# Performance work log

Hardware: AMD Instinct MI355X
Metric: run time of the kernel (lower is better)

The kernel has to match this reference:

```python
import jax, jax.numpy as jnp
import numpy as np

N_NODES = 100_000
N_EDGES = 1_600_000
N_FEAT = 11
HIDDEN = 128
N_GRAPHS = 4096


def gcn_conv(x, W, b, row, col, n_nodes):
    # PyG GCNConv (default): add self-loops, symmetric deg^-1/2 norm,
    # out[col] += norm * (x @ W)[row], then + bias.
    xw = x @ W  # [N, H]
    ew = jnp.ones(row.shape[0], dtype=xw.dtype)
    deg = jax.ops.segment_sum(ew, col, num_segments=n_nodes)
    dis = jnp.where(deg > 0, jax.lax.rsqrt(deg), 0.0).astype(xw.dtype)
    norm = dis[row] * dis[col]  # [E+N]
    msg = xw[row] * norm[:, None]  # gather + scale
    out = jax.ops.segment_sum(msg, col, num_segments=n_nodes)  # scatter-add
    return out + b


def setup_inputs() -> dict:
    key = jax.random.key(0)
    ks = jax.random.split(key, 12)
    x = jax.random.normal(ks[0], (N_NODES, N_FEAT), dtype=jnp.float32)
    edge_index = jax.random.randint(ks[1], (2, N_EDGES), 0, N_NODES, dtype=jnp.int64)
    batch = jnp.sort(jax.random.randint(ks[2], (N_NODES,), 0, N_GRAPHS, dtype=jnp.int64))

    def glorot(k, shape):
        lim = float(np.sqrt(6.0 / (shape[0] + shape[1])))
        return jax.random.uniform(k, shape, jnp.float32, -lim, lim)

    W1 = glorot(ks[3], (N_FEAT, HIDDEN))
    b1 = jnp.zeros((HIDDEN,), jnp.float32)
    W2 = glorot(ks[4], (HIDDEN, HIDDEN))
    b2 = jnp.zeros((HIDDEN,), jnp.float32)
    Wl1 = glorot(ks[5], (HIDDEN, HIDDEN))
    bl1 = jnp.zeros((HIDDEN,), jnp.float32)
    Wl2 = glorot(ks[6], (HIDDEN, 1))
    bl2 = jnp.zeros((1,), jnp.float32)
    return {"x": x, "W1": W1, "b1": b1, "W2": W2, "b2": b2,
            "Wl1": Wl1, "bl1": bl1, "Wl2": Wl2, "bl2": bl2,
            "edge_index": edge_index, "batch": batch}


def reference(x, W1, b1, W2, b2, Wl1, bl1, Wl2, bl2, edge_index, batch):
    n = x.shape[0]
    loops = jnp.arange(n, dtype=edge_index.dtype)
    row = jnp.concatenate([edge_index[0], loops])
    col = jnp.concatenate([edge_index[1], loops])

    h = jax.nn.relu(gcn_conv(x, W1, b1, row, col, n))
    h = jax.nn.relu(gcn_conv(h, W2, b2, row, col, n))

    # global_mean_pool over per-node graph ids
    sums = jax.ops.segment_sum(h, batch, num_segments=N_GRAPHS)
    cnts = jax.ops.segment_sum(jnp.ones((n,), h.dtype), batch, num_segments=N_GRAPHS)
    pooled = sums / jnp.maximum(cnts, 1.0)[:, None]  # [G, H]

    out = jax.nn.relu(pooled @ Wl1 + bl1) @ Wl2 + bl2  # [G, 1]
    return out
```

## Files before the change

### kernel.cpp

```cpp
#include <hip/hip_runtime.h>

#define NN 100000
#define NE 1600000
#define NF 11
#define HID 128
#define NG 4096
#define NB 391

#define BSH 7
#define BNODES 128
#define NBK 782
#define CAP 3072
#define EPB 8192
#define NBB 196

typedef short bf16x8 __attribute__((ext_vector_type(8)));
typedef float f32x4 __attribute__((ext_vector_type(4)));

__device__ __forceinline__ unsigned short f2bf(float f) {
    unsigned u = __float_as_uint(f);
    return (unsigned short)((u + 0x7FFFu + ((u >> 16) & 1u)) >> 16);
}
__device__ __forceinline__ unsigned packbf(float a, float b) {
    return (unsigned)f2bf(a) | ((unsigned)f2bf(b) << 16);
}
__device__ __forceinline__ float bflo(unsigned v) { return __uint_as_float(v << 16); }
__device__ __forceinline__ float bfhi(unsigned v) { return __uint_as_float(v & 0xFFFF0000u); }
__device__ __forceinline__ bf16x8 as_bf(uint4 u) { union { uint4 a; bf16x8 b; } v; v.a = u; return v.b; }

__global__ void k_zero(int* __restrict__ p, int n) {
    int i = blockIdx.x * blockDim.x + threadIdx.x;
    if (i < n) p[i] = 0;
}

__global__ __launch_bounds__(256) void k_bucket(const int* __restrict__ row, const int* __restrict__ col,
                                                int* __restrict__ bcur, int* __restrict__ staging) {
    __shared__ int cnt[NBK];
    __shared__ int loc[NBK];
    const int tid = threadIdx.x;
    const int e0 = blockIdx.x * EPB;
    for (int i = tid; i < NBK; i += 256) { cnt[i] = 0; loc[i] = 0; }
    __syncthreads();
    int rb[32]; unsigned pay[32];
#pragma unroll
    for (int j = 0; j < 32; ++j) {
        int e = e0 + j * 256 + tid;
        int c = (e < NE) ? col[e] : -1;
        int r = (e < NE) ? row[e] : 0;
        rb[j] = (c >= 0) ? (c >> BSH) : -1;
        pay[j] = (unsigned)r | ((unsigned)(c & (BNODES - 1)) << 17);
        if (rb[j] >= 0) atomicAdd(&cnt[rb[j]], 1);
    }
    __syncthreads();
    for (int b = tid; b < NBK; b += 256) {
        int c = cnt[b];
        cnt[b] = (c > 0) ? atomicAdd(&bcur[b], c) : 0;
    }
    __syncthreads();
#pragma unroll
    for (int j = 0; j < 32; ++j) {
        if (rb[j] >= 0) {
            int p = cnt[rb[j]] + atomicAdd(&loc[rb[j]], 1);
            staging[rb[j] * CAP + p] = (int)pay[j];
        }
    }
}

__global__ __launch_bounds__(256) void k_hist2(const int* __restrict__ staging, const int* __restrict__ bcur,
                                               int* __restrict__ degE, float* __restrict__ dis) {
    __shared__ int cnt[BNODES];
    const int b = blockIdx.x, tid = threadIdx.x;
    if (tid < BNODES) cnt[tid] = 0;
    __syncthreads();
    const int sz = bcur[b];
    const int base = b * CAP;
    for (int i = tid; i < sz; i += 256)
        atomicAdd(&cnt[((unsigned)staging[base + i]) >> 17], 1);
    __syncthreads();
    int n = b * BNODES + tid;
    if (tid < BNODES && n < NN) {
        int d = cnt[tid];
        degE[n] = d;
        dis[n] = rsqrtf((float)(d + 1));
    }
}

__global__ void k_scan1(const int* __restrict__ degE, int* __restrict__ startp, int* __restrict__ partial) {
    __shared__ int sh[256];
    int t = threadIdx.x, i = blockIdx.x * 256 + t;
    int v = (i < NN) ? degE[i] : 0;
    sh[t] = v; __syncthreads();
    for (int off = 1; off < 256; off <<= 1) {
        int u = (t >= off) ? sh[t - off] : 0; __syncthreads();
        sh[t] += u; __syncthreads();
    }
    if (i < NN) startp[i] = sh[t] - v;
    if (t == 255) partial[blockIdx.x] = sh[255];
}

__global__ void k_scan2(int* __restrict__ partial) {
    __shared__ int sh[512];
    int t = threadIdx.x;
    int v = (t < NB) ? partial[t] : 0;
    sh[t] = v; __syncthreads();
    for (int off = 1; off < 512; off <<= 1) {
        int u = (t >= off) ? sh[t - off] : 0; __syncthreads();
        sh[t] += u; __syncthreads();
    }
    if (t < NB) partial[t] = sh[t] - v;
}

__global__ void k_scan3(int* __restrict__ startp, const int* __restrict__ partial) {
    int i = blockIdx.x * 256 + threadIdx.x;
    if (i < NN) startp[i] += partial[blockIdx.x];
    if (i == 0) startp[NN] = NE;
}

__global__ __launch_bounds__(256) void k_fillb(const int* __restrict__ staging, const int* __restrict__ bcur,
                                               const int* __restrict__ startp, int* __restrict__ csr) {
    __shared__ int cur[BNODES];
    const int b = blockIdx.x, tid = threadIdx.x;
    int n = b * BNODES + tid;
    if (tid < BNODES) cur[tid] = (n < NN) ? startp[n] : 0;
    __syncthreads();
    const int sz = bcur[b];
    const int base = b * CAP;
    for (int i = tid; i < sz; i += 256) {
        unsigned p = (unsigned)staging[base + i];
        int pos = atomicAdd(&cur[p >> 17], 1);
        csr[pos] = (int)(p & 0x1FFFF);
    }
}

__global__ void k_w2t(const float* __restrict__ W2, unsigned* __restrict__ w2t) {
    int i = blockIdx.x * 256 + threadIdx.x;
    if (i >= HID * 64) return;
    int col = i >> 6, kw = i & 63;
    w2t[col * 64 + kw] = packbf(W2[(2 * kw) * HID + col], W2[(2 * kw + 1) * HID + col]);
}

__global__ __launch_bounds__(256) void k_xd(const float* __restrict__ x, const float* __restrict__ dis,
                                            unsigned* __restrict__ xd8) {
    const int n = blockIdx.x * 16 + (threadIdx.x >> 4);
    const int lane = threadIdx.x & 15;
    float f = (lane < NF) ? x[(size_t)n * NF + lane] : 0.f;
    f *= dis[n];
    float g = __shfl_down(f, 1, 16);
    if ((lane & 1) == 0 && lane < NF)
        xd8[n * 8 + (lane >> 1)] = packbf(f, g);
}

__global__ __launch_bounds__(256) void k_gat1(const unsigned* __restrict__ xd8,
                                              const int* __restrict__ startp,
                                              const int* __restrict__ csr,
                                              float2* __restrict__ aggf2) {
    const int node = blockIdx.x * 4 + (threadIdx.x >> 6);
    const int lane = threadIdx.x & 63;
    const int g = lane >> 3, f = lane & 7;
    const int s = startp[node], e = startp[node + 1];
    float ax = 0.f, ay = 0.f;
    for (int i = s; i < e; i += 64) {
        int idx = (i + lane < e) ? csr[i + lane] : 0;
        int m = e - i;
#pragma unroll
        for (int t = 0; t < 8; ++t) {
            if (t * 8 >= m) break;
            int r = __shfl(idx, t * 8 + g);
            unsigned v = ((t * 8 + g) < m && f < 6) ? xd8[r * 8 + f] : 0u;
            ax += bflo(v); ay += bfhi(v);
        }
    }
    ax += __shfl_xor(ax, 8);  ay += __shfl_xor(ay, 8);
    ax += __shfl_xor(ax, 16); ay += __shfl_xor(ay, 16);
    ax += __shfl_xor(ax, 32); ay += __shfl_xor(ay, 32);
    if (g == 0 && f < 6) {
        unsigned sv = xd8[node * 8 + f];
        aggf2[node * 8 + f] = make_float2(ax + bflo(sv), ay + bfhi(sv));
    }
}

__global__ __launch_bounds__(256) void k_xw1agg(const float2* __restrict__ aggf2, const float* __restrict__ W1,
                                                const float* __restrict__ dis, const float* __restrict__ b1,
                                                unsigned* __restrict__ hb) {
    __shared__ float w1s[NF * HID];
    __shared__ float xs[16 * 16];
    const int tid = threadIdx.x;
    const int n0 = blockIdx.x * 16;
    for (int i = tid; i < NF * HID; i += 256) w1s[i] = W1[i];
    if (tid < 128) {
        int nl = tid >> 3, l = tid & 7;
        if (l < 6) {
            float2 v = aggf2[(size_t)(n0 + nl) * 8 + l];
            xs[nl * 16 + 2 * l] = v.x;
            xs[nl * 16 + 2 * l + 1] = v.y;
        } else {
            xs[nl * 16 + 2 * l] = 0.f;
            xs[nl * 16 + 2 * l + 1] = 0.f;
        }
    }
    __syncthreads();
    const int f2 = tid & 63, sub = tid >> 6;
    float2 bb = ((const float2*)b1)[f2];
#pragma unroll
    for (int p = 0; p < 4; ++p) {
        int nl = p * 4 + sub;
        float s0 = 0.f, s1 = 0.f;
#pragma unroll
        for (int k = 0; k < NF; ++k) {
            float xv = xs[nl * 16 + k];
            s0 = fmaf(xv, w1s[k * HID + f2 * 2], s0);
            s1 = fmaf(xv, w1s[k * HID + f2 * 2 + 1], s1);
        }
        int n = n0 + nl;
        float d = dis[n];
        float ax = fmaxf(fmaf(s0, d, bb.x), 0.f);
        float ay = fmaxf(fmaf(s1, d, bb.y), 0.f);
        hb[n * 64 + f2] = packbf(ax, ay);
    }
}

__global__ __launch_bounds__(256) void k_xw2m(const unsigned* __restrict__ hb,
                                              const unsigned* __restrict__ w2t,
                                              const float* __restrict__ dis,
                                              unsigned* __restrict__ yb) {
    const int tid = threadIdx.x;
    const int wid = tid >> 6, lane = tid & 63;
    const int lr = lane & 15, lk = lane >> 4;
    const int n0 = blockIdx.x * 64;
    const int colb = wid * 32;
    const uint4* h4 = (const uint4*)hb;
    const uint4* w4 = (const uint4*)w2t;

    bf16x8 Bf[2][4];
#pragma unroll
    for (int c = 0; c < 2; ++c)
#pragma unroll
        for (int ks = 0; ks < 4; ++ks)
            Bf[c][ks] = as_bf(w4[(colb + c * 16 + lr) * 16 + ks * 4 + lk]);

    f32x4 acc[4][2];
#pragma unroll
    for (int r = 0; r < 4; ++r)
#pragma unroll
        for (int c = 0; c < 2; ++c) {
            f32x4 z = {0.f, 0.f, 0.f, 0.f};
            acc[r][c] = z;
        }

#pragma unroll
    for (int ks = 0; ks < 4; ++ks) {
        bf16x8 Af[4];
#pragma unroll
        for (int r = 0; r < 4; ++r)
            Af[r] = as_bf(h4[(size_t)(n0 + r * 16 + lr) * 16 + ks * 4 + lk]);
#pragma unroll
        for (int r = 0; r < 4; ++r)
#pragma unroll
            for (int c = 0; c < 2; ++c)
                acc[r][c] = __builtin_amdgcn_mfma_f32_16x16x32_bf16(Af[r], Bf[c][ks], acc[r][c], 0, 0, 0);
    }

#pragma unroll
    for (int r = 0; r < 4; ++r) {
#pragma unroll
        for (int i = 0; i < 4; ++i) {
            int nd = n0 + r * 16 + lk * 4 + i;
            float d = (nd < NN) ? dis[nd] : 0.f;
#pragma unroll
            for (int c = 0; c < 2; ++c) {
                float v = acc[r][c][i] * d;
                float o = __shfl_xor(v, 1);
                if (!(lane & 1) && nd < NN) {
                    int col = colb + c * 16 + lr;
                    yb[nd * 64 + (col >> 1)] = packbf(v, o);
                }
            }
        }
    }
}

__global__ __launch_bounds__(256) void k_gather(const unsigned* __restrict__ yb,
                                                const int* __restrict__ startp,
                                                const int* __restrict__ csr_rows,
                                                const float* __restrict__ dis,
                                                const float* __restrict__ b,
                                                unsigned* __restrict__ hb) {
    const int node = blockIdx.x * 4 + (threadIdx.x >> 6);
    const int lane = threadIdx.x & 63;
    int s = startp[node], e = startp[node + 1];
    unsigned sv = yb[node * 64 + lane];
    float ax = bflo(sv), ay = bfhi(sv);
    for (int i = s; i < e; i += 64) {
        int idx = (i + lane < e) ? csr_rows[i + lane] : 0;
        int m = min(64, e - i);
        int j = 0;
        for (; j + 7 < m; j += 8) {
            unsigned v[8];
#pragma unroll
            for (int u = 0; u < 8; ++u) {
                int r = __shfl(idx, j + u);
                v[u] = yb[r * 64 + lane];
            }
#pragma unroll
            for (int u = 0; u < 8; ++u) { ax += bflo(v[u]); ay += bfhi(v[u]); }
        }
        for (; j + 3 < m; j += 4) {
            unsigned v[4];
#pragma unroll
            for (int u = 0; u < 4; ++u) {
                int r = __shfl(idx, j + u);
                v[u] = yb[r * 64 + lane];
            }
#pragma unroll
            for (int u = 0; u < 4; ++u) { ax += bflo(v[u]); ay += bfhi(v[u]); }
        }
        for (; j < m; ++j) {
            int r = __shfl(idx, j);
            unsigned v = yb[r * 64 + lane];
            ax += bflo(v); ay += bfhi(v);
        }
    }
    float d = dis[node];
    float2 bb = ((const float2*)b)[lane];
    ax = fmaxf(fmaf(ax, d, bb.x), 0.f);
    ay = fmaxf(fmaf(ay, d, bb.y), 0.f);
    hb[node * 64 + lane] = packbf(ax, ay);
}

__global__ void k_bounds(const int* __restrict__ batch, int* __restrict__ gs) {
    int g = blockIdx.x * blockDim.x + threadIdx.x;
    if (g > NG) return;
    int lo = 0, hi = NN;
    while (lo < hi) {
        int mid = (lo + hi) >> 1;
        if (batch[mid] < g) lo = mid + 1; else hi = mid;
    }
    gs[g] = lo;
}

__global__ __launch_bounds__(64) void k_pool(const unsigned* __restrict__ hb, const int* __restrict__ gs,
                                             float* __restrict__ pooled) {
    int g = blockIdx.x, f2 = threadIdx.x;
    int s = gs[g], e = gs[g + 1];
    float ax = 0.f, ay = 0.f;
    for (int n = s; n < e; ++n) {
        unsigned v = hb[(size_t)n * 64 + f2];
        ax += bflo(v); ay += bfhi(v);
    }
    float inv = 1.0f / (float)max(e - s, 1);
    pooled[(size_t)g * HID + f2 * 2] = ax * inv;
    pooled[(size_t)g * HID + f2 * 2 + 1] = ay * inv;
}

__global__ __launch_bounds__(128) void k_head(const float* __restrict__ pooled,
                                              const float* __restrict__ Wl1, const float* __restrict__ bl1,
                                              const float* __restrict__ Wl2, const float* __restrict__ bl2,
                                              float* __restrict__ out) {
    __shared__ float p[HID];
    __shared__ float red[128];
    const int g = blockIdx.x, f = threadIdx.x;
    p[f] = pooled[(size_t)g * HID + f];
    __syncthreads();
    float s = bl1[f];
    for (int k = 0; k < HID; ++k) s = fmaf(p[k], Wl1[k * HID + f], s);
    s = fmaxf(s, 0.f);
    red[f] = s * Wl2[f];
    __syncthreads();
    for (int off = 64; off > 0; off >>= 1) {
        if (f < off) red[f] += red[f + off];
        __syncthreads();
    }
    if (f == 0) out[g] = red[0] + bl2[0];
}

extern "C" void kernel_launch(void* const* d_in, const int* in_sizes, int n_in,
                              void* d_out, int out_size, void* d_ws, size_t ws_size,
                              hipStream_t stream) {
    const float* x   = (const float*)d_in[0];
    const float* W1  = (const float*)d_in[1];
    const float* b1  = (const float*)d_in[2];
    const float* W2  = (const float*)d_in[3];
    const float* b2  = (const float*)d_in[4];
    const float* Wl1 = (const float*)d_in[5];
    const float* bl1 = (const float*)d_in[6];
    const float* Wl2 = (const float*)d_in[7];
    const float* bl2 = (const float*)d_in[8];
    const int* ei    = (const int*)d_in[9];
    const int* batch = (const int*)d_in[10];
    float* out = (float*)d_out;

    const int* row = ei;
    const int* col = ei + NE;

    char* ws = (char*)d_ws;
    size_t off = 0;
    unsigned* yb   = (unsigned*)(ws + off); off += (size_t)NN * 64 * 4;
    unsigned* hb   = (unsigned*)(ws + off); off += (size_t)NN * 64 * 4;
    unsigned* xd8  = (unsigned*)(ws + off); off += (size_t)NN * 8 * 4;
    float2* aggf2  = (float2*)  (ws + off); off += (size_t)NN * 8 * 8;
    int*   degE    = (int*)  (ws + off); off += (size_t)NN * 4;
    float* dis     = (float*)(ws + off); off += (size_t)NN * 4;
    int*   startp  = (int*)  (ws + off); off += (size_t)(NN + 1) * 4;
    int*   partial = (int*)  (ws + off); off += 512 * 4;
    int*   csr     = (int*)  (ws + off); off += (size_t)NE * 4;
    int*   gs      = (int*)  (ws + off); off += (size_t)(NG + 1) * 4;
    float* pooled  = (float*)(ws + off); off += (size_t)NG * HID * 4;
    int*   bcur    = (int*)  (ws + off); off += (size_t)NBK * 4;
    unsigned* w2t  = (unsigned*)(ws + off); off += (size_t)HID * 64 * 4;
    int*   staging = (int*)hb;

    k_zero<<<(NBK + 255) / 256, 256, 0, stream>>>(bcur, NBK);
    k_bucket<<<NBB, 256, 0, stream>>>(row, col, bcur, staging);
    k_hist2<<<NBK, 256, 0, stream>>>(staging, bcur, degE, dis);
    k_scan1<<<NB, 256, 0, stream>>>(degE, startp, partial);
    k_scan2<<<1, 512, 0, stream>>>(partial);
    k_scan3<<<NB, 256, 0, stream>>>(startp, partial);
    k_fillb<<<NBK, 256, 0, stream>>>(staging, bcur, startp, csr);
    k_bounds<<<(NG + 256) / 256, 256, 0, stream>>>(batch, gs);
    k_w2t<<<(HID * 64 + 255) / 256, 256, 0, stream>>>(W2, w2t);

    k_xd<<<NN / 16, 256, 0, stream>>>(x, dis, xd8);
    k_gat1<<<NN / 4, 256, 0, stream>>>(xd8, startp, csr, aggf2);
    k_xw1agg<<<NN / 16, 256, 0, stream>>>(aggf2, W1, dis, b1, hb);

    k_xw2m<<<(NN + 63) / 64, 256, 0, stream>>>(hb, w2t, dis, yb);
    k_gather<<<NN / 4, 256, 0, stream>>>(yb, startp, csr, dis, b2, hb);

    k_pool<<<NG, 64, 0, stream>>>(hb, gs, pooled);
    k_head<<<NG, 128, 0, stream>>>(pooled, Wl1, bl1, Wl2, bl2, out);
}
```

Before: 234.6 us.

## Slice layer-2 features into 8 column slabs for cache-friendly edge gather

The layer-2 message buffer is stored as eight feature slices of 16 columns each (32 bytes per node per slice). The gather now launches eight blocks per node group, one per slice, and each wave handles eight edges at a time with 8 lanes per edge. The intent is to shrink the random-access working set per slice so it fits in L2/MALL, at the cost of reading the CSR indices eight times and issuing 8x more blocks. Layer-1's gather drops its early break in favour of predicated loads, and pooling reads the sliced layout.

```diff
diff --git a/kernel.cpp b/kernel.cpp
--- a/kernel.cpp
+++ b/kernel.cpp
@@ -164,9 +164,9 @@
         int m = e - i;
 #pragma unroll
         for (int t = 0; t < 8; ++t) {
-            if (t * 8 >= m) break;
-            int r = __shfl(idx, t * 8 + g);
-            unsigned v = ((t * 8 + g) < m && f < 6) ? xd8[r * 8 + f] : 0u;
+            int ei = t * 8 + g;
+            int r = __shfl(idx, ei);
+            unsigned v = (ei < m && f < 6) ? xd8[r * 8 + f] : 0u;
             ax += bflo(v); ay += bfhi(v);
         }
     }
@@ -222,7 +222,7 @@
 __global__ __launch_bounds__(256) void k_xw2m(const unsigned* __restrict__ hb,
                                               const unsigned* __restrict__ w2t,
                                               const float* __restrict__ dis,
-                                              unsigned* __restrict__ yb) {
+                                              unsigned* __restrict__ ybs) {
     const int tid = threadIdx.x;
     const int wid = tid >> 6, lane = tid & 63;
     const int lr = lane & 15, lk = lane >> 4;
@@ -271,60 +271,53 @@
                 float v = acc[r][c][i] * d;
                 float o = __shfl_xor(v, 1);
                 if (!(lane & 1) && nd < NN) {
-                    int col = colb + c * 16 + lr;
-                    yb[nd * 64 + (col >> 1)] = packbf(v, o);
+                    int f2 = (colb + c * 16 + lr) >> 1;
+                    ybs[(size_t)(f2 >> 3) * NN * 8 + nd * 8 + (f2 & 7)] = packbf(v, o);
                 }
             }
         }
     }
 }
 
-__global__ __launch_bounds__(256) void k_gather(const unsigned* __restrict__ yb,
-                                                const int* __restrict__ startp,
-                                                const int* __restrict__ csr_rows,
-                                                const float* __restrict__ dis,
-                                                const float* __restrict__ b,
-                                                unsigned* __restrict__ hb) {
-    const int node = blockIdx.x * 4 + (threadIdx.x >> 6);
+__global__ __launch_bounds__(256) void k_gat2s(const unsigned* __restrict__ ybs,
+                                               const int* __restrict__ startp,
+                                               const int* __restrict__ csr,
+                                               const float* __restrict__ dis,
+                                               const float* __restrict__ b2,
+                                               unsigned* __restrict__ hbs) {
+    const int slice = blockIdx.x & 7;
+    const int node = (blockIdx.x >> 3) * 4 + (threadIdx.x >> 6);
     const int lane = threadIdx.x & 63;
-    int s = startp[node], e = startp[node + 1];
-    unsigned sv = yb[node * 64 + lane];
-    float ax = bflo(sv), ay = bfhi(sv);
+    const int g = lane >> 3, f = lane & 7;
+    const unsigned* yb = ybs + (size_t)slice * NN * 8;
+    const int s = __builtin_nontemporal_load(startp + node);
+    const int e = __builtin_nontemporal_load(startp + node + 1);
+    float ax = 0.f, ay = 0.f;
     for (int i = s; i < e; i += 64) {
-        int idx = (i + lane < e) ? csr_rows[i + lane] : 0;
-        int m = min(64, e - i);
-        int j = 0;
-        for (; j + 7 < m; j += 8) {
-            unsigned v[8];
-#pragma unroll
-            for (int u = 0; u < 8; ++u) {
-                int r = __shfl(idx, j + u);
-                v[u] = yb[r * 64 + lane];
-            }
-#pragma unroll
-            for (int u = 0; u < 8; ++u) { ax += bflo(v[u]); ay += bfhi(v[u]); }
-        }
-        for (; j + 3 < m; j += 4) {
-            unsigned v[4];
-#pragma unroll
-            for (int u = 0; u < 4; ++u) {
-                int r = __shfl(idx, j + u);
-                v[u] = yb[r * 64 + lane];
-            }
-#pragma unroll
-            for (int u = 0; u < 4; ++u) { ax += bflo(v[u]); ay += bfhi(v[u]); }
-        }
-        for (; j < m; ++j) {
-            int r = __shfl(idx, j);
-            unsigned v = yb[r * 64 + lane];
+        int idx = 0;
+        if (i + lane < e) idx = __builtin_nontemporal_load(csr + i + lane);
+        int m = e - i;
+#pragma unroll
+        for (int t = 0; t < 8; ++t) {
+            int ei = t * 8 + g;
+            int r = __shfl(idx, ei);
+            unsigned v = (ei < m) ? yb[r * 8 + f] : 0u;
             ax += bflo(v); ay += bfhi(v);
         }
     }
-    float d = dis[node];
-    float2 bb = ((const float2*)b)[lane];
-    ax = fmaxf(fmaf(ax, d, bb.x), 0.f);
-    ay = fmaxf(fmaf(ay, d, bb.y), 0.f);
-    hb[node * 64 + lane] = packbf(ax, ay);
+    ax += __shfl_xor(ax, 8);  ay += __shfl_xor(ay, 8);
+    ax += __shfl_xor(ax, 16); ay += __shfl_xor(ay, 16);
+    ax += __shfl_xor(ax, 32); ay += __shfl_xor(ay, 32);
+    if (g == 0) {
+        unsigned sv = yb[node * 8 + f];
+        ax += bflo(sv); ay += bfhi(sv);
+        float d = dis[node];
+        int f2 = slice * 8 + f;
+        float2 bb = ((const float2*)b2)[f2];
+        ax = fmaxf(fmaf(ax, d, bb.x), 0.f);
+        ay = fmaxf(fmaf(ay, d, bb.y), 0.f);
+        hbs[(size_t)slice * NN * 8 + node * 8 + f] = packbf(ax, ay);
+    }
 }
 
 __global__ void k_bounds(const int* __restrict__ batch, int* __restrict__ gs) {
@@ -338,13 +331,14 @@
     gs[g] = lo;
 }
 
-__global__ __launch_bounds__(64) void k_pool(const unsigned* __restrict__ hb, const int* __restrict__ gs,
+__global__ __launch_bounds__(64) void k_pool(const unsigned* __restrict__ hbs, const int* __restrict__ gs,
                                              float* __restrict__ pooled) {
     int g = blockIdx.x, f2 = threadIdx.x;
     int s = gs[g], e = gs[g + 1];
+    const unsigned* hs = hbs + (size_t)(f2 >> 3) * NN * 8 + (f2 & 7);
     float ax = 0.f, ay = 0.f;
     for (int n = s; n < e; ++n) {
-        unsigned v = hb[(size_t)n * 64 + f2];
+        unsigned v = hs[n * 8];
         ax += bflo(v); ay += bfhi(v);
     }
     float inv = 1.0f / (float)max(e - s, 1);
@@ -394,7 +388,7 @@
 
     char* ws = (char*)d_ws;
     size_t off = 0;
-    unsigned* yb   = (unsigned*)(ws + off); off += (size_t)NN * 64 * 4;
+    unsigned* ybs  = (unsigned*)(ws + off); off += (size_t)NN * 64 * 4;
     unsigned* hb   = (unsigned*)(ws + off); off += (size_t)NN * 64 * 4;
     unsigned* xd8  = (unsigned*)(ws + off); off += (size_t)NN * 8 * 4;
     float2* aggf2  = (float2*)  (ws + off); off += (size_t)NN * 8 * 8;
@@ -408,6 +402,7 @@
     int*   bcur    = (int*)  (ws + off); off += (size_t)NBK * 4;
     unsigned* w2t  = (unsigned*)(ws + off); off += (size_t)HID * 64 * 4;
     int*   staging = (int*)hb;
+    unsigned* hbs  = hb;
 
     k_zero<<<(NBK + 255) / 256, 256, 0, stream>>>(bcur, NBK);
     k_bucket<<<NBB, 256, 0, stream>>>(row, col, bcur, staging);
@@ -423,9 +418,9 @@
     k_gat1<<<NN / 4, 256, 0, stream>>>(xd8, startp, csr, aggf2);
     k_xw1agg<<<NN / 16, 256, 0, stream>>>(aggf2, W1, dis, b1, hb);
 
-    k_xw2m<<<(NN + 63) / 64, 256, 0, stream>>>(hb, w2t, dis, yb);
-    k_gather<<<NN / 4, 256, 0, stream>>>(yb, startp, csr, dis, b2, hb);
-
-    k_pool<<<NG, 64, 0, stream>>>(hb, gs, pooled);
+    k_xw2m<<<(NN + 63) / 64, 256, 0, stream>>>(hb, w2t, dis, ybs);
+    k_gat2s<<<(NN / 4) * 8, 256, 0, stream>>>(ybs, startp, csr, dis, b2, hbs);
+
+    k_pool<<<NG, 64, 0, stream>>>(hbs, gs, pooled);
     k_head<<<NG, 128, 0, stream>>>(pooled, Wl1, bl1, Wl2, bl2, out);
 }
```

Result: slower. 411.8 us (+75.5%).

## Fuse layer-1 transform with layer-2 MFMA matmul via swizzled LDS; retune bucketing

Applied to the files above, without the earlier changes.

Merges the layer-1 feature transform (agg @ W1, bias, ReLU) with the layer-2 bf16 MFMA matmul into a single kernel. The intermediate h1 tile now stays in shared memory with an XOR swizzle instead of being written to and re-read from global memory. It also halves edges per block in the bucketing kernel, doubling the block count, and adds a 16-wide unrolled gather loop for more loads in flight. The costs are more LDS per block (about 25 KB) and higher register pressure from the 16-element unroll.

```diff
diff --git a/kernel.cpp b/kernel.cpp
--- a/kernel.cpp
+++ b/kernel.cpp
@@ -11,8 +11,8 @@
 #define BNODES 128
 #define NBK 782
 #define CAP 3072
-#define EPB 8192
-#define NBB 196
+#define EPB 4096
+#define NBB 391
 
 typedef short bf16x8 __attribute__((ext_vector_type(8)));
 typedef float f32x4 __attribute__((ext_vector_type(4)));
@@ -41,9 +41,9 @@
     const int e0 = blockIdx.x * EPB;
     for (int i = tid; i < NBK; i += 256) { cnt[i] = 0; loc[i] = 0; }
     __syncthreads();
-    int rb[32]; unsigned pay[32];
-#pragma unroll
-    for (int j = 0; j < 32; ++j) {
+    int rb[16]; unsigned pay[16];
+#pragma unroll
+    for (int j = 0; j < 16; ++j) {
         int e = e0 + j * 256 + tid;
         int c = (e < NE) ? col[e] : -1;
         int r = (e < NE) ? row[e] : 0;
@@ -58,7 +58,7 @@
     }
     __syncthreads();
 #pragma unroll
-    for (int j = 0; j < 32; ++j) {
+    for (int j = 0; j < 16; ++j) {
         if (rb[j] >= 0) {
             int p = cnt[rb[j]] + atomicAdd(&loc[rb[j]], 1);
             staging[rb[j] * CAP + p] = (int)pay[j];
@@ -165,8 +165,9 @@
 #pragma unroll
         for (int t = 0; t < 8; ++t) {
             if (t * 8 >= m) break;
-            int r = __shfl(idx, t * 8 + g);
-            unsigned v = ((t * 8 + g) < m && f < 6) ? xd8[r * 8 + f] : 0u;
+            int ei2 = t * 8 + g;
+            int r = __shfl(idx, ei2);
+            unsigned v = (ei2 < m && f < 6) ? xd8[r * 8 + f] : 0u;
             ax += bflo(v); ay += bfhi(v);
         }
     }
@@ -179,31 +180,48 @@
     }
 }
 
-__global__ __launch_bounds__(256) void k_xw1agg(const float2* __restrict__ aggf2, const float* __restrict__ W1,
-                                                const float* __restrict__ dis, const float* __restrict__ b1,
-                                                unsigned* __restrict__ hb) {
+__global__ __launch_bounds__(256) void k_l1l2(const float2* __restrict__ aggf2,
+                                              const float* __restrict__ W1,
+                                              const float* __restrict__ b1,
+                                              const unsigned* __restrict__ w2t,
+                                              const float* __restrict__ dis,
+                                              unsigned* __restrict__ yb) {
     __shared__ float w1s[NF * HID];
-    __shared__ float xs[16 * 16];
+    __shared__ float xs[64 * 16];
+    __shared__ unsigned h1s[64 * 64];
     const int tid = threadIdx.x;
-    const int n0 = blockIdx.x * 16;
+    const int n0 = blockIdx.x * 64;
+    const int wid = tid >> 6, lane = tid & 63;
+    const int lr = lane & 15, lk = lane >> 4;
+    const int colb = wid * 32;
+
     for (int i = tid; i < NF * HID; i += 256) w1s[i] = W1[i];
-    if (tid < 128) {
-        int nl = tid >> 3, l = tid & 7;
-        if (l < 6) {
-            float2 v = aggf2[(size_t)(n0 + nl) * 8 + l];
-            xs[nl * 16 + 2 * l] = v.x;
-            xs[nl * 16 + 2 * l + 1] = v.y;
-        } else {
-            xs[nl * 16 + 2 * l] = 0.f;
-            xs[nl * 16 + 2 * l + 1] = 0.f;
-        }
-    }
-    __syncthreads();
+#pragma unroll
+    for (int p = 0; p < 2; ++p) {
+        int idx = p * 256 + tid;
+        int nl = idx >> 3, l = idx & 7;
+        int n = n0 + nl;
+        float2 v = make_float2(0.f, 0.f);
+        if (l < 6 && n < NN) v = aggf2[(size_t)n * 8 + l];
+        xs[nl * 16 + 2 * l] = v.x;
+        xs[nl * 16 + 2 * l + 1] = v.y;
+    }
+    const uint4* w4 = (const uint4*)w2t;
+    bf16x8 Bf[2][4];
+#pragma unroll
+    for (int c = 0; c < 2; ++c)
+#pragma unroll
+        for (int ks = 0; ks < 4; ++ks)
+            Bf[c][ks] = as_bf(w4[(colb + c * 16 + lr) * 16 + ks * 4 + lk]);
+    __syncthreads();
+
     const int f2 = tid & 63, sub = tid >> 6;
     float2 bb = ((const float2*)b1)[f2];
-#pragma unroll
-    for (int p = 0; p < 4; ++p) {
+    const int jsw = f2 >> 2, ci = f2 & 3;
+#pragma unroll
+    for (int p = 0; p < 16; ++p) {
         int nl = p * 4 + sub;
+        int n = n0 + nl;
         float s0 = 0.f, s1 = 0.f;
 #pragma unroll
         for (int k = 0; k < NF; ++k) {
@@ -211,33 +229,14 @@
             s0 = fmaf(xv, w1s[k * HID + f2 * 2], s0);
             s1 = fmaf(xv, w1s[k * HID + f2 * 2 + 1], s1);
         }
-        int n = n0 + nl;
-        float d = dis[n];
+        float d = (n < NN) ? dis[n] : 0.f;
         float ax = fmaxf(fmaf(s0, d, bb.x), 0.f);
         float ay = fmaxf(fmaf(s1, d, bb.y), 0.f);
-        hb[n * 64 + f2] = packbf(ax, ay);
-    }
-}
-
-__global__ __launch_bounds__(256) void k_xw2m(const unsigned* __restrict__ hb,
-                                              const unsigned* __restrict__ w2t,
-                                              const float* __restrict__ dis,
-                                              unsigned* __restrict__ yb) {
-    const int tid = threadIdx.x;
-    const int wid = tid >> 6, lane = tid & 63;
-    const int lr = lane & 15, lk = lane >> 4;
-    const int n0 = blockIdx.x * 64;
-    const int colb = wid * 32;
-    const uint4* h4 = (const uint4*)hb;
-    const uint4* w4 = (const uint4*)w2t;
-
-    bf16x8 Bf[2][4];
-#pragma unroll
-    for (int c = 0; c < 2; ++c)
-#pragma unroll
-        for (int ks = 0; ks < 4; ++ks)
-            Bf[c][ks] = as_bf(w4[(colb + c * 16 + lr) * 16 + ks * 4 + lk]);
-
+        h1s[nl * 64 + ((jsw ^ (nl & 15)) << 2) + ci] = packbf(ax, ay);
+    }
+    __syncthreads();
+
+    const uint4* h4 = (const uint4*)h1s;
     f32x4 acc[4][2];
 #pragma unroll
     for (int r = 0; r < 4; ++r)
@@ -246,13 +245,12 @@
             f32x4 z = {0.f, 0.f, 0.f, 0.f};
             acc[r][c] = z;
         }
-
 #pragma unroll
     for (int ks = 0; ks < 4; ++ks) {
         bf16x8 Af[4];
 #pragma unroll
         for (int r = 0; r < 4; ++r)
-            Af[r] = as_bf(h4[(size_t)(n0 + r * 16 + lr) * 16 + ks * 4 + lk]);
+            Af[r] = as_bf(h4[(r * 16 + lr) * 16 + ((ks * 4 + lk) ^ lr)]);
 #pragma unroll
         for (int r = 0; r < 4; ++r)
 #pragma unroll
@@ -294,6 +292,16 @@
         int idx = (i + lane < e) ? csr_rows[i + lane] : 0;
         int m = min(64, e - i);
         int j = 0;
+        for (; j + 15 < m; j += 16) {
+            unsigned v[16];
+#pragma unroll
+            for (int u = 0; u < 16; ++u) {
+                int r = __shfl(idx, j + u);
+                v[u] = yb[r * 64 + lane];
+            }
+#pragma unroll
+            for (int u = 0; u < 16; ++u) { ax += bflo(v[u]); ay += bfhi(v[u]); }
+        }
         for (; j + 7 < m; j += 8) {
             unsigned v[8];
 #pragma unroll
@@ -421,9 +429,8 @@
 
     k_xd<<<NN / 16, 256, 0, stream>>>(x, dis, xd8);
     k_gat1<<<NN / 4, 256, 0, stream>>>(xd8, startp, csr, aggf2);
-    k_xw1agg<<<NN / 16, 256, 0, stream>>>(aggf2, W1, dis, b1, hb);
-
-    k_xw2m<<<(NN + 63) / 64, 256, 0, stream>>>(hb, w2t, dis, yb);
+    k_l1l2<<<(NN + 63) / 64, 256, 0, stream>>>(aggf2, W1, b1, w2t, dis, yb);
+
     k_gather<<<NN / 4, 256, 0, stream>>>(yb, startp, csr, dis, b2, hb);
 
     k_pool<<<NG, 64, 0, stream>>>(hb, gs, pooled);
```

After: 220.3 us. 6.1% less time.
